# Kernel tuning notes

Hardware: AMD Instinct MI355X
Metric: run time of the kernel (lower is better)

The kernel has to match this reference:

```python
import jax, jax.numpy as jnp
import numpy as np

N = 100000   # vertices
T = 128      # temporal depth
E = 1600000  # edges (avg degree 16)
K = 9        # conv kernel size
PAD = 4      # 'same' padding -> T preserved
L = 3        # number of layers


def setup_inputs() -> dict:
    key = jax.random.key(0)
    ks = jax.random.split(key, 6)
    x = jax.random.normal(ks[0], (N, T), dtype=jnp.float32)
    edge_index = jax.random.randint(ks[1], (2, E), 0, N, dtype=jnp.int32)
    conv_w = jax.random.normal(ks[2], (L, 1, 1, K), dtype=jnp.float32) * (1.0 / np.sqrt(K))
    conv_b = jax.random.normal(ks[3], (L, 1), dtype=jnp.float32) * 0.1
    W_out = jax.random.normal(ks[4], (3, N), dtype=jnp.float32) * (1.0 / np.sqrt(N))
    b_out = jax.random.normal(ks[5], (3,), dtype=jnp.float32) * 0.1
    return {"x": x, "edge_index": edge_index, "conv_w": conv_w,
            "conv_b": conv_b, "W_out": W_out, "b_out": b_out}


def _conv1d(x, w, b):
    # x: [N, T], w: [1, 1, K] (OIH), b: [1]; torch Conv1d = cross-correlation.
    y = jax.lax.conv_general_dilated(
        x[:, None, :], w, window_strides=(1,), padding=[(PAD, PAD)],
        dimension_numbers=("NCH", "OIH", "NCH"))
    return y[:, 0, :] + b  # [N, T]


def reference(x, edge_index, conv_w, conv_b, W_out, b_out):
    # add_self_loops: append (i, i) for every node
    loop = jnp.arange(N, dtype=edge_index.dtype)
    src = jnp.concatenate([edge_index[0], loop])  # message sources
    dst = jnp.concatenate([edge_index[1], loop])  # aggregation targets
    # in-degree counts (>=1 due to self loops) for mean aggregation
    cnt = jax.ops.segment_sum(jnp.ones(src.shape, jnp.float32), dst,
                              num_segments=N)[:, None]  # [N, 1]
    for i in range(L):
        h = _conv1d(x, conv_w[i], conv_b[i])                    # [N, T]
        s = jax.ops.segment_sum(h[src], dst, num_segments=N)    # scatter-sum of gathered msgs
        x = jax.nn.relu(s / cnt)                                # mean aggr + relu
    x = x.reshape(-1, N)            # [T, N] (row-major view like torch .view)
    return x @ W_out.T + b_out      # [T, 3]
```

## Files before the change

### kernel.cpp

```cpp
#include <hip/hip_runtime.h>

#define NN 100000
#define TT 128
#define EE 1600000
#define KK 9
#define PADK 4
#define NSPLIT 8

#define BSH 9
#define BMASK 511
#define NBUCK 196
#define BCAP 10240

typedef _Float16 f16;
typedef __attribute__((ext_vector_type(2))) _Float16 f16x2;
typedef __attribute__((ext_vector_type(4))) _Float16 f16x4;

union HU { f16x4 h; int2 i; };

__global__ void bin_kernel(const int* __restrict__ ei, int* __restrict__ gcursor,
                           unsigned int* __restrict__ binned) {
    __shared__ int hist[NBUCK];
    __shared__ int gbase[NBUCK];
    int tid = threadIdx.x;
    for (int i = tid; i < NBUCK; i += 256) hist[i] = 0;
    __syncthreads();
    int base = blockIdx.x * 2048;
    unsigned int val[8];
    int bkt[8];
    int rank[8];
#pragma unroll
    for (int k = 0; k < 8; k++) {
        int e = base + k * 256 + tid;
        bkt[k] = -1;
        if (e < EE) {
            int s = ei[e];
            int d = ei[EE + e];
            bkt[k] = d >> BSH;
            val[k] = ((unsigned int)(d & BMASK) << 20) | (unsigned int)s;
            rank[k] = atomicAdd(&hist[bkt[k]], 1);
        }
    }
    __syncthreads();
    for (int i = tid; i < NBUCK; i += 256)
        gbase[i] = hist[i] ? atomicAdd(&gcursor[i], hist[i]) : 0;
    __syncthreads();
#pragma unroll
    for (int k = 0; k < 8; k++) {
        if (bkt[k] >= 0)
            binned[(size_t)bkt[k] * BCAP + gbase[bkt[k]] + rank[k]] = val[k];
    }
}

__global__ void scanpart_kernel(const int* __restrict__ gcursor, int* __restrict__ part,
                                int* __restrict__ offsets) {
    __shared__ int sm[256];
    int tid = threadIdx.x;
    sm[tid] = (tid < NBUCK) ? gcursor[tid] : 0;
    __syncthreads();
    for (int off = 1; off < 256; off <<= 1) {
        int v = (tid >= off) ? sm[tid - off] : 0;
        __syncthreads();
        sm[tid] += v;
        __syncthreads();
    }
    if (tid < NBUCK) part[tid] = (tid == 0) ? 0 : sm[tid - 1];
    if (tid == 0) offsets[NN] = EE;
}

__global__ void bucket_csr_kernel(const unsigned int* __restrict__ binned,
                                  const int* __restrict__ gcursor,
                                  const int* __restrict__ part,
                                  int* __restrict__ offsets,
                                  float* __restrict__ inv_cnt,
                                  int* __restrict__ col) {
    __shared__ int hist[512];
    __shared__ int cur[512];
    __shared__ int sm[256];
    int b = blockIdx.x;
    int tid = threadIdx.x;
    int cnt = gcursor[b];
    const unsigned int* ePtr = binned + (size_t)b * BCAP;
    hist[tid] = 0;
    hist[tid + 256] = 0;
    __syncthreads();
    for (int j = tid; j < cnt; j += 256)
        atomicAdd(&hist[ePtr[j] >> 20], 1);
    __syncthreads();
    int d0 = hist[2 * tid], d1 = hist[2 * tid + 1];
    sm[tid] = d0 + d1;
    __syncthreads();
    for (int off = 1; off < 256; off <<= 1) {
        int v = (tid >= off) ? sm[tid - off] : 0;
        __syncthreads();
        sm[tid] += v;
        __syncthreads();
    }
    int basep = part[b] + ((tid == 0) ? 0 : sm[tid - 1]);
    int node0 = (b << BSH) + 2 * tid;
    int p0 = basep;
    int p1 = basep + d0;
    if (node0 < NN) {
        offsets[node0] = p0;
        inv_cnt[node0] = 1.0f / (1.0f + (float)d0);
        cur[2 * tid] = p0;
    }
    if (node0 + 1 < NN) {
        offsets[node0 + 1] = p1;
        inv_cnt[node0 + 1] = 1.0f / (1.0f + (float)d1);
        cur[2 * tid + 1] = p1;
    }
    __syncthreads();
    for (int j = tid; j < cnt; j += 256) {
        unsigned int v = ePtr[j];
        int pos = atomicAdd(&cur[v >> 20], 1);
        col[pos] = (int)(v & 0xFFFFF);
    }
}

__global__ void cvt_kernel(const float4* __restrict__ x, f16x4* __restrict__ x16) {
    int i = blockIdx.x * blockDim.x + threadIdx.x;
    float4 v = x[i];
    f16x4 o;
    o.x = (f16)v.x; o.y = (f16)v.y; o.z = (f16)v.z; o.w = (f16)v.w;
    x16[i] = o;
}

__global__ void fused_layer_kernel(const f16x4* __restrict__ xin,
                                   const int* __restrict__ offsets,
                                   const int* __restrict__ col,
                                   const float* __restrict__ inv_cnt,
                                   const float* __restrict__ w9,
                                   const float* __restrict__ bptr,
                                   f16x4* __restrict__ yout) {
    int tid = threadIdx.x;
    int lane = tid & 63;
    int half = lane >> 5;
    int p = lane & 31;
    int node = blockIdx.x * 4 + (tid >> 6);

    int lo = offsets[node], hi = offsets[node + 1];
    int cnt = hi - lo;
    int my_col = (lane < cnt) ? col[lo + lane] : 0;
    int jn = cnt < 64 ? cnt : 64;

    const f16 z = (f16)0;
    const f16 hm = half ? (f16)0 : (f16)1;
    f16x4 hmask = {hm, hm, hm, hm};
    f16x4 acc0 = {z, z, z, z};
    f16x4 acc1 = {z, z, z, z};

    int j = 0;
    for (; j + 3 < jn; j += 4) {
        int c0 = __shfl(my_col, j + half);
        int c1 = __shfl(my_col, j + 2 + half);
        f16x4 v0 = xin[(c0 << 5) | p];
        f16x4 v1 = xin[(c1 << 5) | p];
        acc0 += v0;
        acc1 += v1;
    }
    for (; j + 1 < jn; j += 2) {
        int c = __shfl(my_col, j + half);
        acc0 += xin[(c << 5) | p];
    }
    if (j < jn) {
        int c = __shfl(my_col, j);
        acc1 += xin[(c << 5) | p] * hmask;
    }
    for (int k = 64; k < cnt; k++) {
        int c = col[lo + k];
        acc0 += xin[(c << 5) | p] * hmask;
    }
    acc0 += acc1;

    HU u; u.h = acc0;
    int2 o2;
    o2.x = __shfl_xor(u.i.x, 32);
    o2.y = __shfl_xor(u.i.y, 32);
    HU w; w.i = o2;
    acc0 += w.h;

    f16x4 sv = xin[(node << 5) | p];
    float a0 = (float)acc0.x + (float)sv.x;
    float a1 = (float)acc0.y + (float)sv.y;
    float a2 = (float)acc0.z + (float)sv.z;
    float a3 = (float)acc0.w + (float)sv.w;

    float p0 = __shfl_up(a0, 1, 32), p1 = __shfl_up(a1, 1, 32);
    float p2 = __shfl_up(a2, 1, 32), p3 = __shfl_up(a3, 1, 32);
    float n0 = __shfl_down(a0, 1, 32), n1 = __shfl_down(a1, 1, 32);
    float n2 = __shfl_down(a2, 1, 32), n3 = __shfl_down(a3, 1, 32);
    if (p == 0)  { p0 = 0.0f; p1 = 0.0f; p2 = 0.0f; p3 = 0.0f; }
    if (p == 31) { n0 = 0.0f; n1 = 0.0f; n2 = 0.0f; n3 = 0.0f; }

    float w0 = w9[0], w1 = w9[1], w2 = w9[2], w3 = w9[3], w4 = w9[4];
    float w5 = w9[5], w6 = w9[6], w7 = w9[7], w8 = w9[8];
    float s0 = p0*w0 + p1*w1 + p2*w2 + p3*w3 + a0*w4 + a1*w5 + a2*w6 + a3*w7 + n0*w8;
    float s1 = p1*w0 + p2*w1 + p3*w2 + a0*w3 + a1*w4 + a2*w5 + a3*w6 + n0*w7 + n1*w8;
    float s2 = p2*w0 + p3*w1 + a0*w2 + a1*w3 + a2*w4 + a3*w5 + n0*w6 + n1*w7 + n2*w8;
    float s3 = p3*w0 + a0*w1 + a1*w2 + a2*w3 + a3*w4 + n0*w5 + n1*w6 + n2*w7 + n3*w8;

    float ic = inv_cnt[node];
    float b = bptr[0];
    s0 = fmaxf(s0 * ic + b, 0.0f);
    s1 = fmaxf(s1 * ic + b, 0.0f);
    s2 = fmaxf(s2 * ic + b, 0.0f);
    s3 = fmaxf(s3 * ic + b, 0.0f);
    if (half == 0) {
        f16x4 o;
        o.x = (f16)s0; o.y = (f16)s1; o.z = (f16)s2; o.w = (f16)s3;
        yout[(node << 5) | p] = o;
    }
}

__global__ void out_kernel(const f16* __restrict__ y3, const float* __restrict__ Wout,
                           const float* __restrict__ bout, float* __restrict__ out) {
    int t = blockIdx.x;
    int sp = blockIdx.y;
    int tid = threadIdx.x;
    const int per = NN / NSPLIT;
    int lo = sp * per;
    int hi = lo + per;
    float a0 = 0.0f, a1 = 0.0f, a2 = 0.0f;
    for (int n = lo + tid * 2; n < hi; n += 512) {
        f16x2 v2 = *(const f16x2*)(y3 + (size_t)t * NN + n);
        float vx = (float)v2.x, vy = (float)v2.y;
        float2 wA = *(const float2*)(Wout + n);
        float2 wB = *(const float2*)(Wout + NN + n);
        float2 wC = *(const float2*)(Wout + 2 * NN + n);
        a0 += vx * wA.x + vy * wA.y;
        a1 += vx * wB.x + vy * wB.y;
        a2 += vx * wC.x + vy * wC.y;
    }
    for (int o = 32; o > 0; o >>= 1) {
        a0 += __shfl_down(a0, o);
        a1 += __shfl_down(a1, o);
        a2 += __shfl_down(a2, o);
    }
    __shared__ float red[4][3];
    int wave = tid >> 6;
    if ((tid & 63) == 0) {
        red[wave][0] = a0;
        red[wave][1] = a1;
        red[wave][2] = a2;
    }
    __syncthreads();
    if (tid == 0) {
        float r0 = red[0][0] + red[1][0] + red[2][0] + red[3][0];
        float r1 = red[0][1] + red[1][1] + red[2][1] + red[3][1];
        float r2 = red[0][2] + red[1][2] + red[2][2] + red[3][2];
        if (sp == 0) {
            r0 += bout[0];
            r1 += bout[1];
            r2 += bout[2];
        }
        atomicAdd(&out[t * 3 + 0], r0);
        atomicAdd(&out[t * 3 + 1], r1);
        atomicAdd(&out[t * 3 + 2], r2);
    }
}

extern "C" void kernel_launch(void* const* d_in, const int* in_sizes, int n_in,
                              void* d_out, int out_size, void* d_ws, size_t ws_size,
                              hipStream_t stream) {
    const float* x    = (const float*)d_in[0];
    const int*   ei   = (const int*)d_in[1];
    const float* cw   = (const float*)d_in[2];
    const float* cb   = (const float*)d_in[3];
    const float* Wout = (const float*)d_in[4];
    const float* bout = (const float*)d_in[5];
    float* out = (float*)d_out;

    char* ws = (char*)d_ws;
    size_t off = 0;
    auto alloc = [&](size_t bytes) -> void* {
        void* p = ws + off;
        off += (bytes + 255) & ~(size_t)255;
        return p;
    };
    f16*          x16     = (f16*)alloc((size_t)NN * TT * 2);
    f16*          yA      = (f16*)alloc((size_t)NN * TT * 2);
    f16*          yB      = (f16*)alloc((size_t)NN * TT * 2);
    unsigned int* binned  = (unsigned int*)alloc((size_t)NBUCK * BCAP * 4);
    int*          gcursor = (int*)alloc((size_t)NBUCK * 4);
    int*          part    = (int*)alloc((size_t)NBUCK * 4);
    int*          offsets = (int*)alloc((size_t)(NN + 1) * 4);
    float*        inv_cnt = (float*)alloc((size_t)NN * 4);
    int*          col     = (int*)alloc((size_t)EE * 4);

    hipMemsetAsync(gcursor, 0, (size_t)NBUCK * 4, stream);
    bin_kernel<<<(EE + 2047) / 2048, 256, 0, stream>>>(ei, gcursor, binned);
    scanpart_kernel<<<1, 256, 0, stream>>>(gcursor, part, offsets);
    bucket_csr_kernel<<<NBUCK, 256, 0, stream>>>(binned, gcursor, part, offsets, inv_cnt, col);

    cvt_kernel<<<(NN * TT / 4 + 255) / 256, 256, 0, stream>>>((const float4*)x, (f16x4*)x16);

    fused_layer_kernel<<<NN / 4, 256, 0, stream>>>((const f16x4*)x16, offsets, col, inv_cnt,
                                                   cw + 0 * KK, cb + 0, (f16x4*)yA);
    fused_layer_kernel<<<NN / 4, 256, 0, stream>>>((const f16x4*)yA, offsets, col, inv_cnt,
                                                   cw + 1 * KK, cb + 1, (f16x4*)yB);
    fused_layer_kernel<<<NN / 4, 256, 0, stream>>>((const f16x4*)yB, offsets, col, inv_cnt,
                                                   cw + 2 * KK, cb + 2, (f16x4*)yA);

    hipMemsetAsync(out, 0, (size_t)TT * 3 * 4, stream);
    out_kernel<<<dim3(TT, NSPLIT), 256, 0, stream>>>(yA, Wout, bout, out);
}
```

Before: 366.6 us.

## Fuse setup kernels, widen gather to 16-byte loads, restructure output reduction

The fp16 convert is merged into the binning kernel, and the per-bucket scan is folded into the CSR kernel, so two launches go away. The layer kernel now has each lane load 8 halves (16 bytes), so four neighbours are gathered per wave iteration instead of two. The conv uses a 16-lane halo shuffle, and partial sums are combined with two xor reductions. The output GEMV now caches W_out chunks in shared memory and loops over all T per block. That reads W_out once instead of once per timestep, in exchange for more atomics per block.

After: 512.9 us. 39.9% more time.

```diff
diff --git a/kernel.cpp b/kernel.cpp
--- a/kernel.cpp
+++ b/kernel.cpp
@@ -5,24 +5,40 @@
 #define EE 1600000
 #define KK 9
 #define PADK 4
-#define NSPLIT 8
 
 #define BSH 9
 #define BMASK 511
 #define NBUCK 196
 #define BCAP 10240
+#define BINB 782
+#define CVTB 12500
+
+#define OCH 512
+#define ONB 196
 
 typedef _Float16 f16;
 typedef __attribute__((ext_vector_type(2))) _Float16 f16x2;
 typedef __attribute__((ext_vector_type(4))) _Float16 f16x4;
-
-union HU { f16x4 h; int2 i; };
-
-__global__ void bin_kernel(const int* __restrict__ ei, int* __restrict__ gcursor,
-                           unsigned int* __restrict__ binned) {
+typedef __attribute__((ext_vector_type(8))) _Float16 f16x8;
+
+union HU8 { f16x8 h; int4 i; };
+
+__global__ void bin_cvt_kernel(const int* __restrict__ ei, int* __restrict__ gcursor,
+                               unsigned int* __restrict__ binned,
+                               const float4* __restrict__ x, f16x4* __restrict__ x16) {
     __shared__ int hist[NBUCK];
     __shared__ int gbase[NBUCK];
     int tid = threadIdx.x;
+
+    if (blockIdx.x >= BINB) {
+        int i = (blockIdx.x - BINB) * 256 + tid;
+        float4 v = x[i];
+        f16x4 o;
+        o.x = (f16)v.x; o.y = (f16)v.y; o.z = (f16)v.z; o.w = (f16)v.w;
+        x16[i] = o;
+        return;
+    }
+
     for (int i = tid; i < NBUCK; i += 256) hist[i] = 0;
     __syncthreads();
     int base = blockIdx.x * 2048;
@@ -52,25 +68,8 @@
     }
 }
 
-__global__ void scanpart_kernel(const int* __restrict__ gcursor, int* __restrict__ part,
-                                int* __restrict__ offsets) {
-    __shared__ int sm[256];
-    int tid = threadIdx.x;
-    sm[tid] = (tid < NBUCK) ? gcursor[tid] : 0;
-    __syncthreads();
-    for (int off = 1; off < 256; off <<= 1) {
-        int v = (tid >= off) ? sm[tid - off] : 0;
-        __syncthreads();
-        sm[tid] += v;
-        __syncthreads();
-    }
-    if (tid < NBUCK) part[tid] = (tid == 0) ? 0 : sm[tid - 1];
-    if (tid == 0) offsets[NN] = EE;
-}
-
 __global__ void bucket_csr_kernel(const unsigned int* __restrict__ binned,
                                   const int* __restrict__ gcursor,
-                                  const int* __restrict__ part,
                                   int* __restrict__ offsets,
                                   float* __restrict__ inv_cnt,
                                   int* __restrict__ col) {
@@ -79,16 +78,8 @@
     __shared__ int sm[256];
     int b = blockIdx.x;
     int tid = threadIdx.x;
-    int cnt = gcursor[b];
-    const unsigned int* ePtr = binned + (size_t)b * BCAP;
-    hist[tid] = 0;
-    hist[tid + 256] = 0;
-    __syncthreads();
-    for (int j = tid; j < cnt; j += 256)
-        atomicAdd(&hist[ePtr[j] >> 20], 1);
-    __syncthreads();
-    int d0 = hist[2 * tid], d1 = hist[2 * tid + 1];
-    sm[tid] = d0 + d1;
+
+    sm[tid] = (tid < NBUCK) ? gcursor[tid] : 0;
     __syncthreads();
     for (int off = 1; off < 256; off <<= 1) {
         int v = (tid >= off) ? sm[tid - off] : 0;
@@ -96,7 +87,27 @@
         sm[tid] += v;
         __syncthreads();
     }
-    int basep = part[b] + ((tid == 0) ? 0 : sm[tid - 1]);
+    int bucket_base = (b == 0) ? 0 : sm[b - 1];
+    if (b == 0 && tid == 0) offsets[NN] = EE;
+
+    int cnt = gcursor[b];
+    const unsigned int* ePtr = binned + (size_t)b * BCAP;
+    hist[tid] = 0;
+    hist[tid + 256] = 0;
+    __syncthreads();
+    for (int j = tid; j < cnt; j += 256)
+        atomicAdd(&hist[ePtr[j] >> 20], 1);
+    __syncthreads();
+    int d0 = hist[2 * tid], d1 = hist[2 * tid + 1];
+    sm[tid] = d0 + d1;
+    __syncthreads();
+    for (int off = 1; off < 256; off <<= 1) {
+        int v = (tid >= off) ? sm[tid - off] : 0;
+        __syncthreads();
+        sm[tid] += v;
+        __syncthreads();
+    }
+    int basep = bucket_base + ((tid == 0) ? 0 : sm[tid - 1]);
     int node0 = (b << BSH) + 2 * tid;
     int p0 = basep;
     int p1 = basep + d0;
@@ -118,25 +129,17 @@
     }
 }
 
-__global__ void cvt_kernel(const float4* __restrict__ x, f16x4* __restrict__ x16) {
-    int i = blockIdx.x * blockDim.x + threadIdx.x;
-    float4 v = x[i];
-    f16x4 o;
-    o.x = (f16)v.x; o.y = (f16)v.y; o.z = (f16)v.z; o.w = (f16)v.w;
-    x16[i] = o;
-}
-
-__global__ void fused_layer_kernel(const f16x4* __restrict__ xin,
+__global__ void fused_layer_kernel(const f16x8* __restrict__ xin,
                                    const int* __restrict__ offsets,
                                    const int* __restrict__ col,
                                    const float* __restrict__ inv_cnt,
                                    const float* __restrict__ w9,
                                    const float* __restrict__ bptr,
-                                   f16x4* __restrict__ yout) {
+                                   f16x8* __restrict__ yout) {
     int tid = threadIdx.x;
     int lane = tid & 63;
-    int half = lane >> 5;
-    int p = lane & 31;
+    int q = lane >> 4;
+    int p = lane & 15;
     int node = blockIdx.x * 4 + (tid >> 6);
 
     int lo = offsets[node], hi = offsets[node + 1];
@@ -145,118 +148,123 @@
     int jn = cnt < 64 ? cnt : 64;
 
     const f16 z = (f16)0;
-    const f16 hm = half ? (f16)0 : (f16)1;
-    f16x4 hmask = {hm, hm, hm, hm};
-    f16x4 acc0 = {z, z, z, z};
-    f16x4 acc1 = {z, z, z, z};
+    f16x8 acc0 = {z, z, z, z, z, z, z, z};
+    f16x8 acc1 = {z, z, z, z, z, z, z, z};
 
     int j = 0;
-    for (; j + 3 < jn; j += 4) {
-        int c0 = __shfl(my_col, j + half);
-        int c1 = __shfl(my_col, j + 2 + half);
-        f16x4 v0 = xin[(c0 << 5) | p];
-        f16x4 v1 = xin[(c1 << 5) | p];
+    for (; j + 7 < jn; j += 8) {
+        int c0 = __shfl(my_col, j + q);
+        int c1 = __shfl(my_col, j + 4 + q);
+        f16x8 v0 = xin[(c0 << 4) | p];
+        f16x8 v1 = xin[(c1 << 4) | p];
         acc0 += v0;
         acc1 += v1;
     }
-    for (; j + 1 < jn; j += 2) {
-        int c = __shfl(my_col, j + half);
-        acc0 += xin[(c << 5) | p];
+    for (; j + 3 < jn; j += 4) {
+        int c = __shfl(my_col, j + q);
+        acc0 += xin[(c << 4) | p];
     }
     if (j < jn) {
-        int c = __shfl(my_col, j);
-        acc1 += xin[(c << 5) | p] * hmask;
+        int rem = jn - j;
+        int c = __shfl(my_col, j + (q < rem ? q : 0));
+        f16x8 v = xin[(c << 4) | p];
+        if (q < rem) acc1 += v;
     }
     for (int k = 64; k < cnt; k++) {
         int c = col[lo + k];
-        acc0 += xin[(c << 5) | p] * hmask;
+        f16x8 v = xin[(c << 4) | p];
+        if (q == 0) acc0 += v;
     }
     acc0 += acc1;
 
-    HU u; u.h = acc0;
-    int2 o2;
-    o2.x = __shfl_xor(u.i.x, 32);
-    o2.y = __shfl_xor(u.i.y, 32);
-    HU w; w.i = o2;
-    acc0 += w.h;
-
-    f16x4 sv = xin[(node << 5) | p];
-    float a0 = (float)acc0.x + (float)sv.x;
-    float a1 = (float)acc0.y + (float)sv.y;
-    float a2 = (float)acc0.z + (float)sv.z;
-    float a3 = (float)acc0.w + (float)sv.w;
-
-    float p0 = __shfl_up(a0, 1, 32), p1 = __shfl_up(a1, 1, 32);
-    float p2 = __shfl_up(a2, 1, 32), p3 = __shfl_up(a3, 1, 32);
-    float n0 = __shfl_down(a0, 1, 32), n1 = __shfl_down(a1, 1, 32);
-    float n2 = __shfl_down(a2, 1, 32), n3 = __shfl_down(a3, 1, 32);
-    if (p == 0)  { p0 = 0.0f; p1 = 0.0f; p2 = 0.0f; p3 = 0.0f; }
-    if (p == 31) { n0 = 0.0f; n1 = 0.0f; n2 = 0.0f; n3 = 0.0f; }
-
-    float w0 = w9[0], w1 = w9[1], w2 = w9[2], w3 = w9[3], w4 = w9[4];
-    float w5 = w9[5], w6 = w9[6], w7 = w9[7], w8 = w9[8];
-    float s0 = p0*w0 + p1*w1 + p2*w2 + p3*w3 + a0*w4 + a1*w5 + a2*w6 + a3*w7 + n0*w8;
-    float s1 = p1*w0 + p2*w1 + p3*w2 + a0*w3 + a1*w4 + a2*w5 + a3*w6 + n0*w7 + n1*w8;
-    float s2 = p2*w0 + p3*w1 + a0*w2 + a1*w3 + a2*w4 + a3*w5 + n0*w6 + n1*w7 + n2*w8;
-    float s3 = p3*w0 + a0*w1 + a1*w2 + a2*w3 + a3*w4 + n0*w5 + n1*w6 + n2*w7 + n3*w8;
-
+    {
+        HU8 u; u.h = acc0;
+        int4 o;
+        o.x = __shfl_xor(u.i.x, 16); o.y = __shfl_xor(u.i.y, 16);
+        o.z = __shfl_xor(u.i.z, 16); o.w = __shfl_xor(u.i.w, 16);
+        HU8 w; w.i = o;
+        acc0 += w.h;
+        u.h = acc0;
+        o.x = __shfl_xor(u.i.x, 32); o.y = __shfl_xor(u.i.y, 32);
+        o.z = __shfl_xor(u.i.z, 32); o.w = __shfl_xor(u.i.w, 32);
+        w.i = o;
+        acc0 += w.h;
+    }
+
+    f16x8 sv = xin[(node << 4) | p];
+    float A[16];
+    A[4]  = (float)acc0[0] + (float)sv[0];
+    A[5]  = (float)acc0[1] + (float)sv[1];
+    A[6]  = (float)acc0[2] + (float)sv[2];
+    A[7]  = (float)acc0[3] + (float)sv[3];
+    A[8]  = (float)acc0[4] + (float)sv[4];
+    A[9]  = (float)acc0[5] + (float)sv[5];
+    A[10] = (float)acc0[6] + (float)sv[6];
+    A[11] = (float)acc0[7] + (float)sv[7];
+#pragma unroll
+    for (int i = 0; i < 4; i++) {
+        A[i]      = __shfl_up(A[8 + i], 1, 16);
+        A[12 + i] = __shfl_down(A[4 + i], 1, 16);
+    }
+    if (p == 0)  { A[0] = 0.0f; A[1] = 0.0f; A[2] = 0.0f; A[3] = 0.0f; }
+    if (p == 15) { A[12] = 0.0f; A[13] = 0.0f; A[14] = 0.0f; A[15] = 0.0f; }
+
+    float wr[KK];
+#pragma unroll
+    for (int k = 0; k < KK; k++) wr[k] = w9[k];
     float ic = inv_cnt[node];
     float b = bptr[0];
-    s0 = fmaxf(s0 * ic + b, 0.0f);
-    s1 = fmaxf(s1 * ic + b, 0.0f);
-    s2 = fmaxf(s2 * ic + b, 0.0f);
-    s3 = fmaxf(s3 * ic + b, 0.0f);
-    if (half == 0) {
-        f16x4 o;
-        o.x = (f16)s0; o.y = (f16)s1; o.z = (f16)s2; o.w = (f16)s3;
-        yout[(node << 5) | p] = o;
-    }
+    f16x8 o;
+#pragma unroll
+    for (int i = 0; i < 8; i++) {
+        float s = 0.0f;
+#pragma unroll
+        for (int k = 0; k < KK; k++) s += wr[k] * A[i + k];
+        s = fmaxf(s * ic + b, 0.0f);
+        o[i] = (f16)s;
+    }
+    if (q == 0) yout[(node << 4) | p] = o;
 }
 
 __global__ void out_kernel(const f16* __restrict__ y3, const float* __restrict__ Wout,
                            const float* __restrict__ bout, float* __restrict__ out) {
-    int t = blockIdx.x;
-    int sp = blockIdx.y;
+    __shared__ float ws_w[OCH][4];
+    int blk = blockIdx.x;
     int tid = threadIdx.x;
-    const int per = NN / NSPLIT;
-    int lo = sp * per;
-    int hi = lo + per;
-    float a0 = 0.0f, a1 = 0.0f, a2 = 0.0f;
-    for (int n = lo + tid * 2; n < hi; n += 512) {
-        f16x2 v2 = *(const f16x2*)(y3 + (size_t)t * NN + n);
-        float vx = (float)v2.x, vy = (float)v2.y;
-        float2 wA = *(const float2*)(Wout + n);
-        float2 wB = *(const float2*)(Wout + NN + n);
-        float2 wC = *(const float2*)(Wout + 2 * NN + n);
-        a0 += vx * wA.x + vy * wA.y;
-        a1 += vx * wB.x + vy * wB.y;
-        a2 += vx * wC.x + vy * wC.y;
-    }
-    for (int o = 32; o > 0; o >>= 1) {
-        a0 += __shfl_down(a0, o);
-        a1 += __shfl_down(a1, o);
-        a2 += __shfl_down(a2, o);
-    }
-    __shared__ float red[4][3];
+    int n0 = blk * OCH;
+    int chunk = (n0 + OCH <= NN) ? OCH : (NN - n0);
+    for (int i = tid; i < chunk; i += 256) {
+        ws_w[i][0] = Wout[n0 + i];
+        ws_w[i][1] = Wout[NN + n0 + i];
+        ws_w[i][2] = Wout[2 * NN + n0 + i];
+        ws_w[i][3] = 0.0f;
+    }
+    __syncthreads();
     int wave = tid >> 6;
-    if ((tid & 63) == 0) {
-        red[wave][0] = a0;
-        red[wave][1] = a1;
-        red[wave][2] = a2;
-    }
-    __syncthreads();
-    if (tid == 0) {
-        float r0 = red[0][0] + red[1][0] + red[2][0] + red[3][0];
-        float r1 = red[0][1] + red[1][1] + red[2][1] + red[3][1];
-        float r2 = red[0][2] + red[1][2] + red[2][2] + red[3][2];
-        if (sp == 0) {
-            r0 += bout[0];
-            r1 += bout[1];
-            r2 += bout[2];
+    int lane = tid & 63;
+    for (int t = wave; t < TT; t += 4) {
+        float a0 = 0.0f, a1 = 0.0f, a2 = 0.0f;
+        for (int base = lane * 4; base < chunk; base += 256) {
+            f16x4 v = *(const f16x4*)(y3 + (size_t)t * NN + n0 + base);
+#pragma unroll
+            for (int k = 0; k < 4; k++) {
+                float f = (float)v[k];
+                a0 += f * ws_w[base + k][0];
+                a1 += f * ws_w[base + k][1];
+                a2 += f * ws_w[base + k][2];
+            }
         }
-        atomicAdd(&out[t * 3 + 0], r0);
-        atomicAdd(&out[t * 3 + 1], r1);
-        atomicAdd(&out[t * 3 + 2], r2);
+        for (int o = 32; o > 0; o >>= 1) {
+            a0 += __shfl_down(a0, o);
+            a1 += __shfl_down(a1, o);
+            a2 += __shfl_down(a2, o);
+        }
+        if (lane == 0) {
+            if (blk == 0) { a0 += bout[0]; a1 += bout[1]; a2 += bout[2]; }
+            atomicAdd(&out[t * 3 + 0], a0);
+            atomicAdd(&out[t * 3 + 1], a1);
+            atomicAdd(&out[t * 3 + 2], a2);
+        }
     }
 }
 
@@ -283,25 +291,22 @@
     f16*          yB      = (f16*)alloc((size_t)NN * TT * 2);
     unsigned int* binned  = (unsigned int*)alloc((size_t)NBUCK * BCAP * 4);
     int*          gcursor = (int*)alloc((size_t)NBUCK * 4);
-    int*          part    = (int*)alloc((size_t)NBUCK * 4);
     int*          offsets = (int*)alloc((size_t)(NN + 1) * 4);
     float*        inv_cnt = (float*)alloc((size_t)NN * 4);
     int*          col     = (int*)alloc((size_t)EE * 4);
 
     hipMemsetAsync(gcursor, 0, (size_t)NBUCK * 4, stream);
-    bin_kernel<<<(EE + 2047) / 2048, 256, 0, stream>>>(ei, gcursor, binned);
-    scanpart_kernel<<<1, 256, 0, stream>>>(gcursor, part, offsets);
-    bucket_csr_kernel<<<NBUCK, 256, 0, stream>>>(binned, gcursor, part, offsets, inv_cnt, col);
-
-    cvt_kernel<<<(NN * TT / 4 + 255) / 256, 256, 0, stream>>>((const float4*)x, (f16x4*)x16);
-
-    fused_layer_kernel<<<NN / 4, 256, 0, stream>>>((const f16x4*)x16, offsets, col, inv_cnt,
-                                                   cw + 0 * KK, cb + 0, (f16x4*)yA);
-    fused_layer_kernel<<<NN / 4, 256, 0, stream>>>((const f16x4*)yA, offsets, col, inv_cnt,
-                                                   cw + 1 * KK, cb + 1, (f16x4*)yB);
-    fused_layer_kernel<<<NN / 4, 256, 0, stream>>>((const f16x4*)yB, offsets, col, inv_cnt,
-                                                   cw + 2 * KK, cb + 2, (f16x4*)yA);
+    bin_cvt_kernel<<<BINB + CVTB, 256, 0, stream>>>(ei, gcursor, binned,
+                                                    (const float4*)x, (f16x4*)x16);
+    bucket_csr_kernel<<<NBUCK, 256, 0, stream>>>(binned, gcursor, offsets, inv_cnt, col);
+
+    fused_layer_kernel<<<NN / 4, 256, 0, stream>>>((const f16x8*)x16, offsets, col, inv_cnt,
+                                                   cw + 0 * KK, cb + 0, (f16x8*)yA);
+    fused_layer_kernel<<<NN / 4, 256, 0, stream>>>((const f16x8*)yA, offsets, col, inv_cnt,
+                                                   cw + 1 * KK, cb + 1, (f16x8*)yB);
+    fused_layer_kernel<<<NN / 4, 256, 0, stream>>>((const f16x8*)yB, offsets, col, inv_cnt,
+                                                   cw + 2 * KK, cb + 2, (f16x8*)yA);
 
     hipMemsetAsync(out, 0, (size_t)TT * 3 * 4, stream);
-    out_kernel<<<dim3(TT, NSPLIT), 256, 0, stream>>>(yA, Wout, bout, out);
-}
+    out_kernel<<<ONB, 256, 0, stream>>>(yA, Wout, bout, out);
+}
```
